# Performance work log

Hardware: AMD Instinct MI355X
Metric: run time of the kernel (lower is better)

The kernel has to match this reference:

```python
import jax, jax.numpy as jnp
import numpy as np
import math

B, S, E = 4, 4096, 1024
NUM_HEADS = 16
D = E // NUM_HEADS  # attention_size = 64


def setup_inputs() -> dict:
    key = jax.random.key(0)
    ks = jax.random.split(key, 7)
    queries = jax.random.normal(ks[0], (B, S, E), dtype=jnp.float32)
    keys = jax.random.normal(ks[1], (B, S, E), dtype=jnp.float32)
    values = jax.random.normal(ks[2], (B, S, E), dtype=jnp.float32)
    mask = jax.random.randint(ks[3], (B, S, S), 0, 2).astype(bool)
    # nn.Linear(E, D, bias=False): weight [D, E], y = x @ W^T
    lim = 1.0 / math.sqrt(E)
    W_q = jax.random.uniform(ks[4], (D, E), jnp.float32, -lim, lim)
    W_k = jax.random.uniform(ks[5], (D, E), jnp.float32, -lim, lim)
    W_v = jax.random.uniform(ks[6], (D, E), jnp.float32, -lim, lim)
    return {"queries": queries, "keys": keys, "values": values, "mask": mask,
            "W_q": W_q, "W_k": W_k, "W_v": W_v}


def reference(queries, keys, values, mask, W_q, W_k, W_v):
    Q = jnp.einsum('bse,de->bsd', queries, W_q)  # [B,S,D]
    K = jnp.einsum('bse,de->bsd', keys, W_k)
    V = jnp.einsum('bse,de->bsd', values, W_v)
    norm = math.sqrt(D)
    scores = jnp.einsum('bqd,bkd->bqk', Q, K) / norm  # [B,S,S]
    scores = jnp.where(mask, jnp.float32(-1e20), scores)
    attn = jax.nn.softmax(scores, axis=2)
    return jnp.einsum('bqk,bkd->bqd', attn, V)  # [B,S,D]
```

## Files before the change

### kernel.cpp

```cpp
#include <hip/hip_runtime.h>
#include <hip/hip_bf16.h>
#include <math.h>

#define NB 4
#define NS 4096
#define NE 1024
#define ND 64

typedef short bf16x8 __attribute__((ext_vector_type(8)));
typedef float f32x4  __attribute__((ext_vector_type(4)));

__device__ unsigned short g_Wb[3 * ND * NE];
__device__ unsigned short g_Qp[NB * NS * ND];
__device__ unsigned short g_Kp[NB * NS * ND];
__device__ unsigned short g_Vt[NB * ND * NS];
__device__ float g_Po[NB * 64 * 2 * 64 * ND];
__device__ float g_Pl[NB * 64 * 2 * 64];
__device__ int g_flag;

static __device__ inline unsigned short f2bf(float f) {
    __hip_bfloat16 h = __float2bfloat16(f);
    return *reinterpret_cast<unsigned short*>(&h);
}
static __device__ inline unsigned int f2bf2(float lo, float hi) {
    __hip_bfloat162 h = __float22bfloat162_rn(make_float2(lo, hi));
    return *reinterpret_cast<unsigned int*>(&h);
}
static __device__ inline float bf2f(short s) {
    return __uint_as_float(((unsigned int)(unsigned short)s) << 16);
}

#define AS1 __attribute__((address_space(1)))
#define AS3 __attribute__((address_space(3)))
static __device__ __forceinline__ void gll16(const void* g, void* l) {
    __builtin_amdgcn_global_load_lds((const AS1 void*)g, (AS3 void*)l, 16, 0, 0);
}

static __device__ __forceinline__ void lds_barrier() {
    asm volatile("s_waitcnt lgkmcnt(0)" ::: "memory");
    __builtin_amdgcn_s_barrier();
}

__global__ void detect_mask(const unsigned int* __restrict__ mw) {
    __shared__ int found;
    if (threadIdx.x == 0) found = 0;
    __syncthreads();
    int f = 0;
    for (int i = threadIdx.x; i < 4096; i += 256)
        if (mw[i] > 1u) f = 1;
    if (f) atomicOr(&found, 1);
    __syncthreads();
    if (threadIdx.x == 0) g_flag = found;
}

__global__ void prep_w(const float* __restrict__ Wq, const float* __restrict__ Wk,
                       const float* __restrict__ Wv) {
    const int z = blockIdx.x;
    const float* W = (z == 0) ? Wq : (z == 1) ? Wk : Wv;
    unsigned short* o = g_Wb + (size_t)z * (ND * NE);
    const float scale = (z == 0) ? 0.125f : 1.0f;
    int i0 = blockIdx.y * 2048 + threadIdx.x * 8;
    float4 a = *(const float4*)&W[i0];
    float4 b = *(const float4*)&W[i0 + 4];
    ushort4 u0 = { f2bf(a.x * scale), f2bf(a.y * scale), f2bf(a.z * scale), f2bf(a.w * scale) };
    ushort4 u1 = { f2bf(b.x * scale), f2bf(b.y * scale), f2bf(b.z * scale), f2bf(b.w * scale) };
    *(ushort4*)&o[i0]     = u0;
    *(ushort4*)&o[i0 + 4] = u1;
}

__global__ __launch_bounds__(256) void proj_kernel(
    const float* __restrict__ Xq, const float* __restrict__ Xk, const float* __restrict__ Xv)
{
    __shared__ unsigned short Xs[2][64][72];

    const int z = blockIdx.y;
    const float* X = (z == 0) ? Xq : (z == 1) ? Xk : Xv;
    const unsigned short* W = g_Wb + (size_t)z * (ND * NE);

    const int t    = threadIdx.x;
    const int wv   = t >> 6;
    const int lane = t & 63;
    const int quad = lane >> 4;
    const int l16  = lane & 15;
    const int m0   = blockIdx.x * 64;

    const int sr  = t >> 4;
    const int sc4 = (t & 15) * 4;
    const float* Xb = X + (size_t)m0 * NE;

    float4 xr[4][4];

    #pragma unroll
    for (int d = 0; d < 4; ++d)
        #pragma unroll
        for (int p = 0; p < 4; ++p)
            xr[d][p] = *(const float4*)&Xb[(size_t)(sr + p * 16) * NE + d * 64 + sc4];
    #pragma unroll
    for (int p = 0; p < 4; ++p) {
        uint2 u = { f2bf2(xr[0][p].x, xr[0][p].y), f2bf2(xr[0][p].z, xr[0][p].w) };
        *(uint2*)&Xs[0][sr + p * 16][sc4] = u;
    }
    lds_barrier();

    f32x4 acc[4] = {};

    #pragma unroll
    for (int c = 0; c < 16; ++c) {
        if (c + 4 < 16) {
            #pragma unroll
            for (int p = 0; p < 4; ++p)
                xr[c & 3][p] = *(const float4*)&Xb[(size_t)(sr + p * 16) * NE + (c + 4) * 64 + sc4];
        }

        #pragma unroll
        for (int ks = 0; ks < 2; ++ks) {
            bf16x8 a = *(const bf16x8*)&Xs[c & 1][wv * 16 + l16][ks * 32 + quad * 8];
            #pragma unroll
            for (int nt = 0; nt < 4; ++nt) {
                bf16x8 bb = *(const bf16x8*)&W[(size_t)(nt * 16 + l16) * NE + c * 64 + ks * 32 + quad * 8];
                acc[nt] = __builtin_amdgcn_mfma_f32_16x16x32_bf16(a, bb, acc[nt], 0, 0, 0);
            }
        }

        if (c + 1 < 16) {
            #pragma unroll
            for (int p = 0; p < 4; ++p) {
                float4 v = xr[(c + 1) & 3][p];
                uint2 u = { f2bf2(v.x, v.y), f2bf2(v.z, v.w) };
                *(uint2*)&Xs[(c + 1) & 1][sr + p * 16][sc4] = u;
            }
        }
        lds_barrier();
    }

    unsigned short (*T)[68] = (unsigned short(*)[68])&Xs[0][0][0];

    if (z == 2) {
        #pragma unroll
        for (int nt = 0; nt < 4; ++nt)
            #pragma unroll
            for (int r = 0; r < 4; ++r)
                T[nt * 16 + l16][wv * 16 + quad * 4 + r] = f2bf(acc[nt][r]);
    } else {
        #pragma unroll
        for (int nt = 0; nt < 4; ++nt)
            #pragma unroll
            for (int r = 0; r < 4; ++r)
                T[wv * 16 + quad * 4 + r][nt * 16 + l16] = f2bf(acc[nt][r]);
    }
    lds_barrier();

    {
        const int dr  = t >> 2;
        const int c16 = (t & 3) * 16;
        uint4 u0 = *(const uint4*)&T[dr][c16];
        uint4 u1 = *(const uint4*)&T[dr][c16 + 8];
        if (z == 2) {
            const int bb = m0 >> 12, s0 = m0 & 4095;
            unsigned short* dst = g_Vt + ((size_t)bb * ND + dr) * NS + s0 + c16;
            *(uint4*)&dst[0] = u0;
            *(uint4*)&dst[8] = u1;
        } else {
            unsigned short* dst = (z == 0 ? g_Qp : g_Kp) + (size_t)(m0 + dr) * ND + c16;
            *(uint4*)&dst[0] = u0;
            *(uint4*)&dst[8] = u1;
        }
    }
}

__global__ __launch_bounds__(256) void attn_kernel(
    const void* __restrict__ maskp)
{
    __shared__ unsigned short KT[2][64 * 64];
    __shared__ unsigned short VT[2][64 * 64];
    __shared__ unsigned char  MR[4][4][1024];
    __shared__ short          Ss[4][16][72];

    const int t    = threadIdx.x;
    const int wv   = t >> 6;
    const int lane = t & 63;
    const int quad = lane >> 4;
    const int l16  = lane & 15;

    const int n    = blockIdx.x;
    const int xcd  = n & 7;
    const int b    = xcd >> 1;
    const int kh   = xcd & 1;
    const int qt   = n >> 3;
    const int q0   = qt * 64;
    const int wq0  = q0 + wv * 16;
    const int koff = kh * 2048;

    const bool m_u8 = (g_flag != 0);
    const unsigned char* m8  = (const unsigned char*)maskp;
    const int*           m32 = (const int*)maskp;

    const unsigned short* Qrow = g_Qp + ((size_t)b * NS + wq0 + l16) * ND;
    const bf16x8 qf0 = *(const bf16x8*)&Qrow[quad * 8];
    const bf16x8 qf1 = *(const bf16x8*)&Qrow[32 + quad * 8];

    const unsigned short* Kbase = g_Kp + ((size_t)b * NS) * ND;
    const unsigned short* Vbase = g_Vt + (size_t)b * ND * NS;

    const int r8 = lane >> 3;
    const int c8 = lane & 7;
    const int sw = c8 ^ r8;

    const unsigned char* m8k =
        m8 + ((size_t)b * NS + wq0 + (lane >> 2)) * (size_t)NS + koff + (lane & 3) * 16;

    float l_row = 0.0f;
    f32x4 Oacc[4] = {};

    const int rsw = l16 & 7;

    if (m_u8) {
        #pragma unroll
        for (int j = 0; j < 2; ++j) {
            const int row = wv * 16 + j * 8 + r8;
            gll16(Kbase + ((size_t)koff + row) * 64 + sw * 8, &KT[0][(wv * 16 + j * 8) * 64]);
            gll16(Vbase + (size_t)row * NS + koff + sw * 8, &VT[0][(wv * 16 + j * 8) * 64]);
        }
        gll16(m8k, &MR[0][wv][0]);
        gll16(m8k + 64, &MR[1][wv][0]);
        asm volatile("s_waitcnt vmcnt(1)" ::: "memory");
        __builtin_amdgcn_s_barrier();

        #pragma unroll 2
        for (int it = 0; it < 32; ++it) {
            const int buf = it & 1;
            const int k0  = koff + it * 64;

            if (it < 31) {
                const int k1 = k0 + 64;
                #pragma unroll
                for (int j = 0; j < 2; ++j) {
                    const int row = wv * 16 + j * 8 + r8;
                    gll16(Kbase + (size_t)(k1 + row) * 64 + sw * 8,
                          &KT[buf ^ 1][(wv * 16 + j * 8) * 64]);
                    gll16(Vbase + (size_t)row * NS + k1 + sw * 8,
                          &VT[buf ^ 1][(wv * 16 + j * 8) * 64]);
                }
            }
            if (it < 30)
                gll16(m8k + (it + 2) * 64, &MR[(it + 2) & 3][wv][0]);

            f32x4 sc[4] = {};
            __builtin_amdgcn_s_setprio(1);
            #pragma unroll
            for (int kt = 0; kt < 4; ++kt) {
                const int row = kt * 16 + l16;
                bf16x8 kf0 = *(const bf16x8*)&KT[buf][row * 64 + ((quad ^ rsw) << 3)];
                bf16x8 kf1 = *(const bf16x8*)&KT[buf][row * 64 + (((4 + quad) ^ rsw) << 3)];
                sc[kt] = __builtin_amdgcn_mfma_f32_16x16x32_bf16(qf0, kf0, sc[kt], 0, 0, 0);
                sc[kt] = __builtin_amdgcn_mfma_f32_16x16x32_bf16(qf1, kf1, sc[kt], 0, 0, 0);
            }
            __builtin_amdgcn_s_setprio(0);

            #pragma unroll
            for (int kt = 0; kt < 4; ++kt)
                #pragma unroll
                for (int r = 0; r < 4; ++r)
                    Ss[wv][quad * 4 + r][kt * 16 + l16] = (short)f2bf(__expf(sc[kt][r]));

            asm volatile("s_waitcnt lgkmcnt(0)" ::: "memory");

            bf16x8 a0 = *(const bf16x8*)&Ss[wv][l16][quad * 8];
            bf16x8 a1 = *(const bf16x8*)&Ss[wv][l16][32 + quad * 8];
            {
                const unsigned char* MRt = &MR[it & 3][wv][0];
                uint2 mm0 = *(const uint2*)&MRt[l16 * 64 + quad * 8];
                uint2 mm1 = *(const uint2*)&MRt[l16 * 64 + 32 + quad * 8];
                #pragma unroll
                for (int j = 0; j < 4; ++j) {
                    a0[j]     = ((mm0.x >> (8 * j)) & 255u) ? (short)0 : a0[j];
                    a0[4 + j] = ((mm0.y >> (8 * j)) & 255u) ? (short)0 : a0[4 + j];
                    a1[j]     = ((mm1.x >> (8 * j)) & 255u) ? (short)0 : a1[j];
                    a1[4 + j] = ((mm1.y >> (8 * j)) & 255u) ? (short)0 : a1[4 + j];
                }
            }
            {
                float ls = 0.0f;
                #pragma unroll
                for (int j = 0; j < 8; ++j) ls += bf2f(a0[j]) + bf2f(a1[j]);
                l_row += ls;
            }
            __builtin_amdgcn_s_setprio(1);
            #pragma unroll
            for (int nt = 0; nt < 4; ++nt) {
                const int row = nt * 16 + l16;
                bf16x8 vf0 = *(const bf16x8*)&VT[buf][row * 64 + ((quad ^ rsw) << 3)];
                bf16x8 vf1 = *(const bf16x8*)&VT[buf][row * 64 + (((4 + quad) ^ rsw) << 3)];
                Oacc[nt] = __builtin_amdgcn_mfma_f32_16x16x32_bf16(a0, vf0, Oacc[nt], 0, 0, 0);
                Oacc[nt] = __builtin_amdgcn_mfma_f32_16x16x32_bf16(a1, vf1, Oacc[nt], 0, 0, 0);
            }
            __builtin_amdgcn_s_setprio(0);

            if (it < 31) {
                if (it < 30) asm volatile("s_waitcnt vmcnt(1)" ::: "memory");
                else         asm volatile("s_waitcnt vmcnt(0)" ::: "memory");
                __builtin_amdgcn_s_barrier();
            }
        }
    } else {
        #pragma unroll
        for (int j = 0; j < 2; ++j) {
            const int row = wv * 16 + j * 8 + r8;
            gll16(Kbase + ((size_t)koff + row) * 64 + sw * 8, &KT[0][(wv * 16 + j * 8) * 64]);
            gll16(Vbase + (size_t)row * NS + koff + sw * 8, &VT[0][(wv * 16 + j * 8) * 64]);
        }
        asm volatile("s_waitcnt vmcnt(0)" ::: "memory");
        __builtin_amdgcn_s_barrier();

        #pragma unroll 2
        for (int it = 0; it < 32; ++it) {
            const int buf = it & 1;
            const int k0  = koff + it * 64;

            if (it < 31) {
                const int k1 = k0 + 64;
                #pragma unroll
                for (int j = 0; j < 2; ++j) {
                    const int row = wv * 16 + j * 8 + r8;
                    gll16(Kbase + (size_t)(k1 + row) * 64 + sw * 8,
                          &KT[buf ^ 1][(wv * 16 + j * 8) * 64]);
                    gll16(Vbase + (size_t)row * NS + k1 + sw * 8,
                          &VT[buf ^ 1][(wv * 16 + j * 8) * 64]);
                }
            }

            f32x4 sc[4] = {};
            #pragma unroll
            for (int kt = 0; kt < 4; ++kt) {
                const int row = kt * 16 + l16;
                bf16x8 kf0 = *(const bf16x8*)&KT[buf][row * 64 + ((quad ^ rsw) << 3)];
                bf16x8 kf1 = *(const bf16x8*)&KT[buf][row * 64 + (((4 + quad) ^ rsw) << 3)];
                sc[kt] = __builtin_amdgcn_mfma_f32_16x16x32_bf16(qf0, kf0, sc[kt], 0, 0, 0);
                sc[kt] = __builtin_amdgcn_mfma_f32_16x16x32_bf16(qf1, kf1, sc[kt], 0, 0, 0);
            }

            #pragma unroll
            for (int r = 0; r < 4; ++r) {
                size_t mrow = ((size_t)b * NS + (wq0 + quad * 4 + r)) * (size_t)NS + k0;
                #pragma unroll
                for (int kt = 0; kt < 4; ++kt) {
                    int mv = m32[mrow + kt * 16 + l16];
                    float p = mv ? 0.0f : __expf(sc[kt][r]);
                    Ss[wv][quad * 4 + r][kt * 16 + l16] = (short)f2bf(p);
                }
            }

            asm volatile("s_waitcnt lgkmcnt(0)" ::: "memory");

            bf16x8 a0 = *(const bf16x8*)&Ss[wv][l16][quad * 8];
            bf16x8 a1 = *(const bf16x8*)&Ss[wv][l16][32 + quad * 8];
            {
                float ls = 0.0f;
                #pragma unroll
                for (int j = 0; j < 8; ++j) ls += bf2f(a0[j]) + bf2f(a1[j]);
                l_row += ls;
            }
            #pragma unroll
            for (int nt = 0; nt < 4; ++nt) {
                const int row = nt * 16 + l16;
                bf16x8 vf0 = *(const bf16x8*)&VT[buf][row * 64 + ((quad ^ rsw) << 3)];
                bf16x8 vf1 = *(const bf16x8*)&VT[buf][row * 64 + (((4 + quad) ^ rsw) << 3)];
                Oacc[nt] = __builtin_amdgcn_mfma_f32_16x16x32_bf16(a0, vf0, Oacc[nt], 0, 0, 0);
                Oacc[nt] = __builtin_amdgcn_mfma_f32_16x16x32_bf16(a1, vf1, Oacc[nt], 0, 0, 0);
            }

            if (it < 31) {
                asm volatile("s_waitcnt vmcnt(0)" ::: "memory");
                __builtin_amdgcn_s_barrier();
            }
        }
    }

    l_row += __shfl_xor(l_row, 16);
    l_row += __shfl_xor(l_row, 32);

    float* po = g_Po + ((((size_t)b * 64 + qt) * 2 + kh) * 64) * 64;
    #pragma unroll
    for (int r = 0; r < 4; ++r) {
        const int ql = wv * 16 + quad * 4 + r;
        #pragma unroll
        for (int nt = 0; nt < 4; ++nt)
            po[(size_t)ql * 64 + nt * 16 + l16] = Oacc[nt][r];
    }
    if (quad == 0)
        g_Pl[(((size_t)b * 64 + qt) * 2 + kh) * 64 + wv * 16 + l16] = l_row;
}

__global__ __launch_bounds__(256) void merge_kernel(float* __restrict__ out) {
    const int tid = blockIdx.x * 256 + threadIdx.x;
    const int r   = tid >> 4;
    const int d4  = (tid & 15) * 4;
    const int b = r >> 12, s = r & 4095, qt = s >> 6, ql = s & 63;
    const size_t base = ((size_t)b * 64 + qt) * 2;
    const float* p0 = g_Po + ((base + 0) * 64 + ql) * 64 + d4;
    const float* p1 = g_Po + ((base + 1) * 64 + ql) * 64 + d4;
    f32x4 a = *(const f32x4*)p0;
    f32x4 c = *(const f32x4*)p1;
    float l = g_Pl[(base + 0) * 64 + ql] + g_Pl[(base + 1) * 64 + ql];
    float inv = 1.0f / l;
    f32x4 o = (a + c) * inv;
    *(f32x4*)&out[(size_t)r * ND + d4] = o;
}

extern "C" void kernel_launch(void* const* d_in, const int* in_sizes, int n_in,
                              void* d_out, int out_size, void* d_ws, size_t ws_size,
                              hipStream_t stream) {
    const float* queries = (const float*)d_in[0];
    const float* keys    = (const float*)d_in[1];
    const float* values  = (const float*)d_in[2];
    const void*  mask    = d_in[3];
    const float* Wq      = (const float*)d_in[4];
    const float* Wk      = (const float*)d_in[5];
    const float* Wv      = (const float*)d_in[6];
    float* out = (float*)d_out;

    hipLaunchKernelGGL(detect_mask, dim3(1), dim3(256), 0, stream,
                       (const unsigned int*)mask);
    hipLaunchKernelGGL(prep_w, dim3(3, 32), dim3(256), 0, stream, Wq, Wk, Wv);
    hipLaunchKernelGGL(proj_kernel, dim3((NB * NS) / 64, 3), dim3(256), 0, stream,
                       queries, keys, values);
    hipLaunchKernelGGL(attn_kernel, dim3(512), dim3(256), 0, stream, mask);
    hipLaunchKernelGGL(merge_kernel, dim3(1024), dim3(256), 0, stream, out);
}
```

Measured before the change: 536.7 us.

## Triple-buffer attention K/V, stage projection weights in LDS, fold log2e, MFMA row sums

The attention loop moves from double to triple buffering of K/V tiles, prefetching two tiles ahead with a relaxed vmcnt wait so loads overlap compute. The projection kernel stages weight tiles through swizzled LDS with async global-to-LDS loads instead of reading W straight from global memory for every MFMA. The log2(e) factor is folded into the Q weight scale so exp2f replaces __expf. The row-sum reduction is now done by an MFMA against a vector of ones instead of scalar bf16 conversions and shuffles. In exchange the kernels use more LDS, which may lower occupancy, and the last iterations issue redundant clamped loads.

After: 528.7 us. About the same (-1.5%).

```diff
diff --git a/kernel.cpp b/kernel.cpp
--- a/kernel.cpp
+++ b/kernel.cpp
@@ -26,19 +26,11 @@
     __hip_bfloat162 h = __float22bfloat162_rn(make_float2(lo, hi));
     return *reinterpret_cast<unsigned int*>(&h);
 }
-static __device__ inline float bf2f(short s) {
-    return __uint_as_float(((unsigned int)(unsigned short)s) << 16);
-}
 
 #define AS1 __attribute__((address_space(1)))
 #define AS3 __attribute__((address_space(3)))
 static __device__ __forceinline__ void gll16(const void* g, void* l) {
     __builtin_amdgcn_global_load_lds((const AS1 void*)g, (AS3 void*)l, 16, 0, 0);
-}
-
-static __device__ __forceinline__ void lds_barrier() {
-    asm volatile("s_waitcnt lgkmcnt(0)" ::: "memory");
-    __builtin_amdgcn_s_barrier();
 }
 
 __global__ void detect_mask(const unsigned int* __restrict__ mw) {
@@ -58,7 +50,7 @@
     const int z = blockIdx.x;
     const float* W = (z == 0) ? Wq : (z == 1) ? Wk : Wv;
     unsigned short* o = g_Wb + (size_t)z * (ND * NE);
-    const float scale = (z == 0) ? 0.125f : 1.0f;
+    const float scale = (z == 0) ? 0.125f * 1.4426950408889634f : 1.0f;
     int i0 = blockIdx.y * 2048 + threadIdx.x * 8;
     float4 a = *(const float4*)&W[i0];
     float4 b = *(const float4*)&W[i0 + 4];
@@ -72,6 +64,7 @@
     const float* __restrict__ Xq, const float* __restrict__ Xk, const float* __restrict__ Xv)
 {
     __shared__ unsigned short Xs[2][64][72];
+    __shared__ unsigned short Ws[4][64 * 64];
 
     const int z = blockIdx.y;
     const float* X = (z == 0) ? Xq : (z == 1) ? Xk : Xv;
@@ -83,13 +76,25 @@
     const int quad = lane >> 4;
     const int l16  = lane & 15;
     const int m0   = blockIdx.x * 64;
+    const int rsw  = l16 & 7;
 
     const int sr  = t >> 4;
     const int sc4 = (t & 15) * 4;
     const float* Xb = X + (size_t)m0 * NE;
 
+    const int wrow = t >> 3;
+    const int wch  = t & 7;
+
     float4 xr[4][4];
 
+    #pragma unroll
+    for (int d = 0; d < 2; ++d)
+        #pragma unroll
+        for (int j = 0; j < 2; ++j) {
+            const int row = j * 32 + wrow;
+            gll16(W + (size_t)row * NE + d * 64 + ((wch ^ (row & 7)) << 3),
+                  &Ws[d][j * 2048 + wv * 512]);
+        }
     #pragma unroll
     for (int d = 0; d < 4; ++d)
         #pragma unroll
@@ -100,24 +105,62 @@
         uint2 u = { f2bf2(xr[0][p].x, xr[0][p].y), f2bf2(xr[0][p].z, xr[0][p].w) };
         *(uint2*)&Xs[0][sr + p * 16][sc4] = u;
     }
-    lds_barrier();
+    asm volatile("s_waitcnt vmcnt(0) lgkmcnt(0)" ::: "memory");
+    __builtin_amdgcn_s_barrier();
 
     f32x4 acc[4] = {};
 
     #pragma unroll
-    for (int c = 0; c < 16; ++c) {
-        if (c + 4 < 16) {
-            #pragma unroll
-            for (int p = 0; p < 4; ++p)
-                xr[c & 3][p] = *(const float4*)&Xb[(size_t)(sr + p * 16) * NE + (c + 4) * 64 + sc4];
-        }
+    for (int c = 0; c < 12; ++c) {
+        #pragma unroll
+        for (int j = 0; j < 2; ++j) {
+            const int row = j * 32 + wrow;
+            gll16(W + (size_t)row * NE + (c + 2) * 64 + ((wch ^ (row & 7)) << 3),
+                  &Ws[(c + 2) & 3][j * 2048 + wv * 512]);
+        }
+        #pragma unroll
+        for (int p = 0; p < 4; ++p)
+            xr[c & 3][p] = *(const float4*)&Xb[(size_t)(sr + p * 16) * NE + (c + 4) * 64 + sc4];
 
         #pragma unroll
         for (int ks = 0; ks < 2; ++ks) {
             bf16x8 a = *(const bf16x8*)&Xs[c & 1][wv * 16 + l16][ks * 32 + quad * 8];
             #pragma unroll
             for (int nt = 0; nt < 4; ++nt) {
-                bf16x8 bb = *(const bf16x8*)&W[(size_t)(nt * 16 + l16) * NE + c * 64 + ks * 32 + quad * 8];
+                const int row = nt * 16 + l16;
+                bf16x8 bb = *(const bf16x8*)&Ws[c & 3][row * 64 + (((ks * 4 + quad) ^ rsw) << 3)];
+                acc[nt] = __builtin_amdgcn_mfma_f32_16x16x32_bf16(a, bb, acc[nt], 0, 0, 0);
+            }
+        }
+
+        #pragma unroll
+        for (int p = 0; p < 4; ++p) {
+            float4 v = xr[(c + 1) & 3][p];
+            uint2 u = { f2bf2(v.x, v.y), f2bf2(v.z, v.w) };
+            *(uint2*)&Xs[(c + 1) & 1][sr + p * 16][sc4] = u;
+        }
+        asm volatile("s_waitcnt vmcnt(6) lgkmcnt(0)" ::: "memory");
+        __builtin_amdgcn_s_barrier();
+    }
+
+    #pragma unroll
+    for (int c = 12; c < 16; ++c) {
+        if (c + 2 < 16) {
+            #pragma unroll
+            for (int j = 0; j < 2; ++j) {
+                const int row = j * 32 + wrow;
+                gll16(W + (size_t)row * NE + (c + 2) * 64 + ((wch ^ (row & 7)) << 3),
+                      &Ws[(c + 2) & 3][j * 2048 + wv * 512]);
+            }
+        }
+
+        #pragma unroll
+        for (int ks = 0; ks < 2; ++ks) {
+            bf16x8 a = *(const bf16x8*)&Xs[c & 1][wv * 16 + l16][ks * 32 + quad * 8];
+            #pragma unroll
+            for (int nt = 0; nt < 4; ++nt) {
+                const int row = nt * 16 + l16;
+                bf16x8 bb = *(const bf16x8*)&Ws[c & 3][row * 64 + (((ks * 4 + quad) ^ rsw) << 3)];
                 acc[nt] = __builtin_amdgcn_mfma_f32_16x16x32_bf16(a, bb, acc[nt], 0, 0, 0);
             }
         }
@@ -130,7 +173,8 @@
                 *(uint2*)&Xs[(c + 1) & 1][sr + p * 16][sc4] = u;
             }
         }
-        lds_barrier();
+        asm volatile("s_waitcnt vmcnt(0) lgkmcnt(0)" ::: "memory");
+        __builtin_amdgcn_s_barrier();
     }
 
     unsigned short (*T)[68] = (unsigned short(*)[68])&Xs[0][0][0];
@@ -148,7 +192,8 @@
             for (int r = 0; r < 4; ++r)
                 T[wv * 16 + quad * 4 + r][nt * 16 + l16] = f2bf(acc[nt][r]);
     }
-    lds_barrier();
+    asm volatile("s_waitcnt lgkmcnt(0)" ::: "memory");
+    __builtin_amdgcn_s_barrier();
 
     {
         const int dr  = t >> 2;
@@ -171,8 +216,8 @@
 __global__ __launch_bounds__(256) void attn_kernel(
     const void* __restrict__ maskp)
 {
-    __shared__ unsigned short KT[2][64 * 64];
-    __shared__ unsigned short VT[2][64 * 64];
+    __shared__ unsigned short KT[3][64 * 64];
+    __shared__ unsigned short VT[3][64 * 64];
     __shared__ unsigned char  MR[4][4][1024];
     __shared__ short          Ss[4][16][72];
 
@@ -187,8 +232,7 @@
     const int b    = xcd >> 1;
     const int kh   = xcd & 1;
     const int qt   = n >> 3;
-    const int q0   = qt * 64;
-    const int wq0  = q0 + wv * 16;
+    const int wq0  = qt * 64 + wv * 16;
     const int koff = kh * 2048;
 
     const bool m_u8 = (g_flag != 0);
@@ -205,53 +249,54 @@
     const int r8 = lane >> 3;
     const int c8 = lane & 7;
     const int sw = c8 ^ r8;
+    const int rsw = l16 & 7;
 
     const unsigned char* m8k =
         m8 + ((size_t)b * NS + wq0 + (lane >> 2)) * (size_t)NS + koff + (lane & 3) * 16;
 
-    float l_row = 0.0f;
+    bf16x8 ones;
+    #pragma unroll
+    for (int j = 0; j < 8; ++j) ones[j] = (short)0x3F80;
+
+    f32x4 lsum = {};
     f32x4 Oacc[4] = {};
 
-    const int rsw = l16 & 7;
-
     if (m_u8) {
         #pragma unroll
-        for (int j = 0; j < 2; ++j) {
-            const int row = wv * 16 + j * 8 + r8;
-            gll16(Kbase + ((size_t)koff + row) * 64 + sw * 8, &KT[0][(wv * 16 + j * 8) * 64]);
-            gll16(Vbase + (size_t)row * NS + koff + sw * 8, &VT[0][(wv * 16 + j * 8) * 64]);
-        }
-        gll16(m8k, &MR[0][wv][0]);
-        gll16(m8k + 64, &MR[1][wv][0]);
-        asm volatile("s_waitcnt vmcnt(1)" ::: "memory");
+        for (int d = 0; d < 2; ++d) {
+            const int kg = koff + d * 64;
+            #pragma unroll
+            for (int j = 0; j < 2; ++j) {
+                const int row = wv * 16 + j * 8 + r8;
+                gll16(Kbase + (size_t)(kg + row) * 64 + sw * 8, &KT[d][(wv * 16 + j * 8) * 64]);
+                gll16(Vbase + (size_t)row * NS + kg + sw * 8, &VT[d][(wv * 16 + j * 8) * 64]);
+            }
+            gll16(m8k + d * 64, &MR[d][wv][0]);
+        }
+        asm volatile("s_waitcnt vmcnt(0)" ::: "memory");
         __builtin_amdgcn_s_barrier();
 
-        #pragma unroll 2
+        int sR = 0, sW = 2;
         for (int it = 0; it < 32; ++it) {
-            const int buf = it & 1;
-            const int k0  = koff + it * 64;
-
-            if (it < 31) {
-                const int k1 = k0 + 64;
-                #pragma unroll
-                for (int j = 0; j < 2; ++j) {
-                    const int row = wv * 16 + j * 8 + r8;
-                    gll16(Kbase + (size_t)(k1 + row) * 64 + sw * 8,
-                          &KT[buf ^ 1][(wv * 16 + j * 8) * 64]);
-                    gll16(Vbase + (size_t)row * NS + k1 + sw * 8,
-                          &VT[buf ^ 1][(wv * 16 + j * 8) * 64]);
-                }
-            }
-            if (it < 30)
-                gll16(m8k + (it + 2) * 64, &MR[(it + 2) & 3][wv][0]);
-
+            const int kc = (it + 2 < 32) ? it + 2 : 31;
+            const int kg = koff + kc * 64;
+            #pragma unroll
+            for (int j = 0; j < 2; ++j) {
+                const int row = wv * 16 + j * 8 + r8;
+                gll16(Kbase + (size_t)(kg + row) * 64 + sw * 8, &KT[sW][(wv * 16 + j * 8) * 64]);
+                gll16(Vbase + (size_t)row * NS + kg + sw * 8, &VT[sW][(wv * 16 + j * 8) * 64]);
+            }
+            gll16(m8k + kc * 64, &MR[(it + 2) & 3][wv][0]);
+
+            const unsigned short* KTs = &KT[sR][0];
+            const unsigned short* VTs = &VT[sR][0];
             f32x4 sc[4] = {};
             __builtin_amdgcn_s_setprio(1);
             #pragma unroll
             for (int kt = 0; kt < 4; ++kt) {
                 const int row = kt * 16 + l16;
-                bf16x8 kf0 = *(const bf16x8*)&KT[buf][row * 64 + ((quad ^ rsw) << 3)];
-                bf16x8 kf1 = *(const bf16x8*)&KT[buf][row * 64 + (((4 + quad) ^ rsw) << 3)];
+                bf16x8 kf0 = *(const bf16x8*)&KTs[row * 64 + ((quad ^ rsw) << 3)];
+                bf16x8 kf1 = *(const bf16x8*)&KTs[row * 64 + (((4 + quad) ^ rsw) << 3)];
                 sc[kt] = __builtin_amdgcn_mfma_f32_16x16x32_bf16(qf0, kf0, sc[kt], 0, 0, 0);
                 sc[kt] = __builtin_amdgcn_mfma_f32_16x16x32_bf16(qf1, kf1, sc[kt], 0, 0, 0);
             }
@@ -261,7 +306,7 @@
             for (int kt = 0; kt < 4; ++kt)
                 #pragma unroll
                 for (int r = 0; r < 4; ++r)
-                    Ss[wv][quad * 4 + r][kt * 16 + l16] = (short)f2bf(__expf(sc[kt][r]));
+                    Ss[wv][quad * 4 + r][kt * 16 + l16] = (short)f2bf(exp2f(sc[kt][r]));
 
             asm volatile("s_waitcnt lgkmcnt(0)" ::: "memory");
 
@@ -279,73 +324,70 @@
                     a1[4 + j] = ((mm1.y >> (8 * j)) & 255u) ? (short)0 : a1[4 + j];
                 }
             }
-            {
-                float ls = 0.0f;
-                #pragma unroll
-                for (int j = 0; j < 8; ++j) ls += bf2f(a0[j]) + bf2f(a1[j]);
-                l_row += ls;
-            }
+
             __builtin_amdgcn_s_setprio(1);
+            lsum = __builtin_amdgcn_mfma_f32_16x16x32_bf16(a0, ones, lsum, 0, 0, 0);
+            lsum = __builtin_amdgcn_mfma_f32_16x16x32_bf16(a1, ones, lsum, 0, 0, 0);
             #pragma unroll
             for (int nt = 0; nt < 4; ++nt) {
                 const int row = nt * 16 + l16;
-                bf16x8 vf0 = *(const bf16x8*)&VT[buf][row * 64 + ((quad ^ rsw) << 3)];
-                bf16x8 vf1 = *(const bf16x8*)&VT[buf][row * 64 + (((4 + quad) ^ rsw) << 3)];
+                bf16x8 vf0 = *(const bf16x8*)&VTs[row * 64 + ((quad ^ rsw) << 3)];
+                bf16x8 vf1 = *(const bf16x8*)&VTs[row * 64 + (((4 + quad) ^ rsw) << 3)];
                 Oacc[nt] = __builtin_amdgcn_mfma_f32_16x16x32_bf16(a0, vf0, Oacc[nt], 0, 0, 0);
                 Oacc[nt] = __builtin_amdgcn_mfma_f32_16x16x32_bf16(a1, vf1, Oacc[nt], 0, 0, 0);
             }
             __builtin_amdgcn_s_setprio(0);
 
-            if (it < 31) {
-                if (it < 30) asm volatile("s_waitcnt vmcnt(1)" ::: "memory");
-                else         asm volatile("s_waitcnt vmcnt(0)" ::: "memory");
-                __builtin_amdgcn_s_barrier();
-            }
+            asm volatile("s_waitcnt vmcnt(5) lgkmcnt(0)" ::: "memory");
+            __builtin_amdgcn_s_barrier();
+            sR = (sR == 2) ? 0 : sR + 1;
+            sW = (sW == 2) ? 0 : sW + 1;
         }
     } else {
         #pragma unroll
-        for (int j = 0; j < 2; ++j) {
-            const int row = wv * 16 + j * 8 + r8;
-            gll16(Kbase + ((size_t)koff + row) * 64 + sw * 8, &KT[0][(wv * 16 + j * 8) * 64]);
-            gll16(Vbase + (size_t)row * NS + koff + sw * 8, &VT[0][(wv * 16 + j * 8) * 64]);
+        for (int d = 0; d < 2; ++d) {
+            const int kg = koff + d * 64;
+            #pragma unroll
+            for (int j = 0; j < 2; ++j) {
+                const int row = wv * 16 + j * 8 + r8;
+                gll16(Kbase + (size_t)(kg + row) * 64 + sw * 8, &KT[d][(wv * 16 + j * 8) * 64]);
+                gll16(Vbase + (size_t)row * NS + kg + sw * 8, &VT[d][(wv * 16 + j * 8) * 64]);
+            }
         }
         asm volatile("s_waitcnt vmcnt(0)" ::: "memory");
         __builtin_amdgcn_s_barrier();
 
-        #pragma unroll 2
+        int sR = 0, sW = 2;
         for (int it = 0; it < 32; ++it) {
-            const int buf = it & 1;
-            const int k0  = koff + it * 64;
-
-            if (it < 31) {
-                const int k1 = k0 + 64;
-                #pragma unroll
-                for (int j = 0; j < 2; ++j) {
-                    const int row = wv * 16 + j * 8 + r8;
-                    gll16(Kbase + (size_t)(k1 + row) * 64 + sw * 8,
-                          &KT[buf ^ 1][(wv * 16 + j * 8) * 64]);
-                    gll16(Vbase + (size_t)row * NS + k1 + sw * 8,
-                          &VT[buf ^ 1][(wv * 16 + j * 8) * 64]);
-                }
-            }
-
+            const int kc = (it + 2 < 32) ? it + 2 : 31;
+            const int kg = koff + kc * 64;
+            #pragma unroll
+            for (int j = 0; j < 2; ++j) {
+                const int row = wv * 16 + j * 8 + r8;
+                gll16(Kbase + (size_t)(kg + row) * 64 + sw * 8, &KT[sW][(wv * 16 + j * 8) * 64]);
+                gll16(Vbase + (size_t)row * NS + kg + sw * 8, &VT[sW][(wv * 16 + j * 8) * 64]);
+            }
+
+            const unsigned short* KTs = &KT[sR][0];
+            const unsigned short* VTs = &VT[sR][0];
             f32x4 sc[4] = {};
             #pragma unroll
             for (int kt = 0; kt < 4; ++kt) {
                 const int row = kt * 16 + l16;
-                bf16x8 kf0 = *(const bf16x8*)&KT[buf][row * 64 + ((quad ^ rsw) << 3)];
-                bf16x8 kf1 = *(const bf16x8*)&KT[buf][row * 64 + (((4 + quad) ^ rsw) << 3)];
+                bf16x8 kf0 = *(const bf16x8*)&KTs[row * 64 + ((quad ^ rsw) << 3)];
+                bf16x8 kf1 = *(const bf16x8*)&KTs[row * 64 + (((4 + quad) ^ rsw) << 3)];
                 sc[kt] = __builtin_amdgcn_mfma_f32_16x16x32_bf16(qf0, kf0, sc[kt], 0, 0, 0);
                 sc[kt] = __builtin_amdgcn_mfma_f32_16x16x32_bf16(qf1, kf1, sc[kt], 0, 0, 0);
             }
 
+            const int k0 = koff + it * 64;
             #pragma unroll
             for (int r = 0; r < 4; ++r) {
                 size_t mrow = ((size_t)b * NS + (wq0 + quad * 4 + r)) * (size_t)NS + k0;
                 #pragma unroll
                 for (int kt = 0; kt < 4; ++kt) {
                     int mv = m32[mrow + kt * 16 + l16];
-                    float p = mv ? 0.0f : __expf(sc[kt][r]);
+                    float p = mv ? 0.0f : exp2f(sc[kt][r]);
                     Ss[wv][quad * 4 + r][kt * 16 + l16] = (short)f2bf(p);
                 }
             }
@@ -354,30 +396,23 @@
 
             bf16x8 a0 = *(const bf16x8*)&Ss[wv][l16][quad * 8];
             bf16x8 a1 = *(const bf16x8*)&Ss[wv][l16][32 + quad * 8];
-            {
-                float ls = 0.0f;
-                #pragma unroll
-                for (int j = 0; j < 8; ++j) ls += bf2f(a0[j]) + bf2f(a1[j]);
-                l_row += ls;
-            }
+            lsum = __builtin_amdgcn_mfma_f32_16x16x32_bf16(a0, ones, lsum, 0, 0, 0);
+            lsum = __builtin_amdgcn_mfma_f32_16x16x32_bf16(a1, ones, lsum, 0, 0, 0);
             #pragma unroll
             for (int nt = 0; nt < 4; ++nt) {
                 const int row = nt * 16 + l16;
-                bf16x8 vf0 = *(const bf16x8*)&VT[buf][row * 64 + ((quad ^ rsw) << 3)];
-                bf16x8 vf1 = *(const bf16x8*)&VT[buf][row * 64 + (((4 + quad) ^ rsw) << 3)];
+                bf16x8 vf0 = *(const bf16x8*)&VTs[row * 64 + ((quad ^ rsw) << 3)];
+                bf16x8 vf1 = *(const bf16x8*)&VTs[row * 64 + (((4 + quad) ^ rsw) << 3)];
                 Oacc[nt] = __builtin_amdgcn_mfma_f32_16x16x32_bf16(a0, vf0, Oacc[nt], 0, 0, 0);
                 Oacc[nt] = __builtin_amdgcn_mfma_f32_16x16x32_bf16(a1, vf1, Oacc[nt], 0, 0, 0);
             }
 
-            if (it < 31) {
-                asm volatile("s_waitcnt vmcnt(0)" ::: "memory");
-                __builtin_amdgcn_s_barrier();
-            }
-        }
-    }
-
-    l_row += __shfl_xor(l_row, 16);
-    l_row += __shfl_xor(l_row, 32);
+            asm volatile("s_waitcnt vmcnt(0) lgkmcnt(0)" ::: "memory");
+            __builtin_amdgcn_s_barrier();
+            sR = (sR == 2) ? 0 : sR + 1;
+            sW = (sW == 2) ? 0 : sW + 1;
+        }
+    }
 
     float* po = g_Po + ((((size_t)b * 64 + qt) * 2 + kh) * 64) * 64;
     #pragma unroll
@@ -387,8 +422,12 @@
         for (int nt = 0; nt < 4; ++nt)
             po[(size_t)ql * 64 + nt * 16 + l16] = Oacc[nt][r];
     }
-    if (quad == 0)
-        g_Pl[(((size_t)b * 64 + qt) * 2 + kh) * 64 + wv * 16 + l16] = l_row;
+    if (l16 == 0) {
+        #pragma unroll
+        for (int r = 0; r < 4; ++r)
+            g_Pl[(((size_t)b * 64 + qt) * 2 + kh) * 64 + wv * 16 + quad * 4 + r] = lsum[r];
+    }
+    asm volatile("s_waitcnt vmcnt(0)" ::: "memory");
 }
 
 __global__ __launch_bounds__(256) void merge_kernel(float* __restrict__ out) {
```
